# Kernel optimization log

Hardware: AMD Instinct MI355X
Metric: run time of the kernel (lower is better)

## Reference

```python
import jax, jax.numpy as jnp
import numpy as np

HIDDEN = 4544
NUM_HEADS = 71
HEAD_DIM = 64
SEQ = 2048
ROPE_BASE = 10000.0


def setup_inputs() -> dict:
    key = jax.random.key(0)
    k1, k2, k3 = jax.random.split(key, 3)
    hidden_states = jax.random.normal(k1, (1, 1, SEQ, HIDDEN), dtype=jnp.float32)
    # additive causal mask (0 on/below diagonal, -1e9 above)
    causal = jnp.tril(jnp.ones((SEQ, SEQ), dtype=bool))
    attention_mask = jnp.where(causal, 0.0, -1e9).astype(jnp.float32)[None, None]
    w_qkv = jax.random.normal(k2, (HIDDEN, (NUM_HEADS + 2) * HEAD_DIM), dtype=jnp.float32) * 0.02
    w_dense = jax.random.normal(k3, (HIDDEN, HIDDEN), dtype=jnp.float32) * 0.02
    # RoPE caches as in TtFalconRotaryEmbedding
    inv_freq = 1.0 / (ROPE_BASE ** (jnp.arange(0, HEAD_DIM, 2, dtype=jnp.float32) / HEAD_DIM))
    t = jnp.arange(SEQ, dtype=jnp.float32)
    freqs = jnp.outer(t, inv_freq)                      # [S, HD/2]
    emb = jnp.concatenate([freqs, freqs], axis=-1)      # [S, HD]
    return {
        "hidden_states": hidden_states,
        "attention_mask": attention_mask,
        "w_qkv": w_qkv,
        "w_dense": w_dense,
        "cos": jnp.cos(emb),
        "sin": jnp.sin(emb),
    }


def _rope(x, cos, sin):
    # x: [..., S, HD]; Falcon rotate_half: cat(-x2, x1)
    x1, x2 = jnp.split(x, 2, axis=-1)
    rot = jnp.concatenate([-x2, x1], axis=-1)
    return x * cos + rot * sin


def reference(hidden_states, attention_mask, w_qkv, w_dense, cos, sin):
    S = hidden_states.shape[2]
    x = hidden_states[0, 0]                              # [S, H]
    qkv = (x @ w_qkv).reshape(S, NUM_HEADS + 2, HEAD_DIM)
    q = jnp.transpose(qkv[:, :NUM_HEADS], (1, 0, 2))     # [nh, S, hd]
    k = qkv[:, NUM_HEADS]                                # [S, hd] (single MQA K head)
    v = qkv[:, NUM_HEADS + 1]                            # [S, hd]
    q = _rope(q, cos[None, :S], sin[None, :S])
    k = _rope(k, cos[:S], sin[:S])
    scale = 1.0 / np.sqrt(HEAD_DIM).astype(np.float32)
    scores = jnp.einsum('hsd,td->hst', q, k) * scale + attention_mask[0, 0][None]
    probs = jax.nn.softmax(scores, axis=-1)              # [nh, S, S]
    ctx = jnp.einsum('hst,td->hsd', probs, v)            # [nh, S, hd]
    out = jnp.transpose(ctx, (1, 0, 2)).reshape(S, NUM_HEADS * HEAD_DIM) @ w_dense
    return out[None, None]                               # [1, 1, S, H]
```

## Files before the change

### kernel.cpp

```cpp
#include <hip/hip_runtime.h>

typedef unsigned short u16;
typedef unsigned int u32;
typedef __attribute__((ext_vector_type(8))) __bf16 bf16x8;
typedef __attribute__((ext_vector_type(4))) float f32x4;

#define SEQ   2048
#define NH    71
#define HD    64
#define HID   4544
#define NQKV  4672
#define KP    4608

__device__ __forceinline__ u16 f2bf(float f) {
    __bf16 b = (__bf16)f;
    return __builtin_bit_cast(u16, b);
}

__device__ __forceinline__ void gload_lds16(const u16* g, u16* l) {
    __builtin_amdgcn_global_load_lds(
        (const __attribute__((address_space(1))) u32*)g,
        (__attribute__((address_space(3))) u32*)l, 16, 0, 0);
}

__global__ __launch_bounds__(256) void k_convert(const float* __restrict__ in,
                                                 u16* __restrict__ out) {
    const int row = blockIdx.x;
    const float* src = in + (size_t)row * HID;
    u16* dst = out + (size_t)row * KP;
    for (int c = threadIdx.x; c < KP / 8; c += 256) {
        u16 o[8];
        if (c < HID / 8) {
            float4 v0 = *(const float4*)(src + c * 8);
            float4 v1 = *(const float4*)(src + c * 8 + 4);
            o[0] = f2bf(v0.x); o[1] = f2bf(v0.y); o[2] = f2bf(v0.z); o[3] = f2bf(v0.w);
            o[4] = f2bf(v1.x); o[5] = f2bf(v1.y); o[6] = f2bf(v1.z); o[7] = f2bf(v1.w);
        } else {
#pragma unroll
            for (int j = 0; j < 8; ++j) o[j] = 0;
        }
        *(uint4*)(dst + c * 8) = *(uint4*)o;
    }
}

__global__ __launch_bounds__(256) void k_transpose(const float* __restrict__ in,
                                                   u16* __restrict__ out,
                                                   int R, int C, int Rp) {
    __shared__ float tile[32][33];
    int c0 = blockIdx.x * 32, r0 = blockIdx.y * 32;
    int tx = threadIdx.x & 31, ty = threadIdx.x >> 5;
#pragma unroll
    for (int i = 0; i < 32; i += 8) {
        int r = r0 + ty + i, c = c0 + tx;
        tile[ty + i][tx] = (r < R && c < C) ? in[(size_t)r * C + c] : 0.f;
    }
    __syncthreads();
#pragma unroll
    for (int i = 0; i < 32; i += 8)
        out[(size_t)(c0 + ty + i) * Rp + r0 + tx] = f2bf(tile[tx][ty + i]);
}

__global__ __launch_bounds__(512, 2) void k_gemm256(const u16* __restrict__ A,
                                                    const u16* __restrict__ BT,
                                                    float* __restrict__ C,
                                                    int N, int ldc) {
    __shared__ u16 lsA[2][256 * 64];
    __shared__ u16 lsB[2][256 * 64];
    const int tid = threadIdx.x;
    const int lane = tid & 63;
    const int wid = tid >> 6;
    const int wr = wid >> 2, wc = wid & 3;
    const int l15 = lane & 15, lg = lane >> 4;

    const int lin = blockIdx.y * gridDim.x + blockIdx.x;
    const int m0 = (lin & 7) * 256;
    const int n0 = (lin >> 3) * 256;

    const int srow = tid >> 3, sc = tid & 7;
    const u16* Ag = A + (size_t)(m0 + srow) * KP + (sc ^ (srow & 7)) * 8;
    const u16* Bg = BT + (size_t)(n0 + srow) * KP + (sc ^ (srow & 7)) * 8;

    f32x4 acc[8][4];
#pragma unroll
    for (int i = 0; i < 8; ++i)
#pragma unroll
        for (int j = 0; j < 4; ++j) acc[i][j] = (f32x4){0.f, 0.f, 0.f, 0.f};

#define STAGE(d, t)                                                                  \
    do {                                                                             \
        const size_t ko = (size_t)(t) * 64;                                          \
        _Pragma("unroll") for (int j = 0; j < 4; ++j)                                \
            gload_lds16(Ag + (size_t)j * 64 * KP + ko,                               \
                        lsA[d] + (j * 64 + srow) * 64 + sc * 8);                     \
        _Pragma("unroll") for (int j = 0; j < 4; ++j)                                \
            gload_lds16(Bg + (size_t)j * 64 * KP + ko,                               \
                        lsB[d] + (j * 64 + srow) * 64 + sc * 8);                     \
    } while (0)

    STAGE(0, 0);
    __syncthreads();

    const int NT = KP / 64;
    for (int t = 0; t < NT; ++t) {
        const int d = t & 1;
        if (t + 1 < NT) STAGE(d ^ 1, t + 1);
        const u16* La = lsA[d];
        const u16* Lb = lsB[d];
        bf16x8 bfr[4], af[4];
#pragma unroll
        for (int ni = 0; ni < 4; ++ni) {
            int r = wc * 64 + ni * 16 + l15;
            bfr[ni] = *(const bf16x8*)(Lb + r * 64 + ((lg ^ (r & 7)) << 3));
        }
#pragma unroll
        for (int mi = 0; mi < 4; ++mi) {
            int r = wr * 128 + mi * 16 + l15;
            af[mi] = *(const bf16x8*)(La + r * 64 + ((lg ^ (r & 7)) << 3));
        }
        __builtin_amdgcn_s_setprio(1);
#pragma unroll
        for (int mi = 0; mi < 4; ++mi)
#pragma unroll
            for (int ni = 0; ni < 4; ++ni)
                acc[mi][ni] = __builtin_amdgcn_mfma_f32_16x16x32_bf16(
                    af[mi], bfr[ni], acc[mi][ni], 0, 0, 0);
        __builtin_amdgcn_s_setprio(0);
        __builtin_amdgcn_s_barrier();
#pragma unroll
        for (int mi = 0; mi < 4; ++mi) {
            int r = wr * 128 + (mi + 4) * 16 + l15;
            af[mi] = *(const bf16x8*)(La + r * 64 + ((lg ^ (r & 7)) << 3));
        }
        __builtin_amdgcn_s_setprio(1);
#pragma unroll
        for (int mi = 0; mi < 4; ++mi)
#pragma unroll
            for (int ni = 0; ni < 4; ++ni)
                acc[mi + 4][ni] = __builtin_amdgcn_mfma_f32_16x16x32_bf16(
                    af[mi], bfr[ni], acc[mi + 4][ni], 0, 0, 0);
        __builtin_amdgcn_s_setprio(0);
        __builtin_amdgcn_s_barrier();
#pragma unroll
        for (int ni = 0; ni < 4; ++ni) {
            int r = wc * 64 + ni * 16 + l15;
            bfr[ni] = *(const bf16x8*)(Lb + r * 64 + (((4 + lg) ^ (r & 7)) << 3));
        }
#pragma unroll
        for (int mi = 0; mi < 4; ++mi) {
            int r = wr * 128 + mi * 16 + l15;
            af[mi] = *(const bf16x8*)(La + r * 64 + (((4 + lg) ^ (r & 7)) << 3));
        }
        __builtin_amdgcn_s_setprio(1);
#pragma unroll
        for (int mi = 0; mi < 4; ++mi)
#pragma unroll
            for (int ni = 0; ni < 4; ++ni)
                acc[mi][ni] = __builtin_amdgcn_mfma_f32_16x16x32_bf16(
                    af[mi], bfr[ni], acc[mi][ni], 0, 0, 0);
        __builtin_amdgcn_s_setprio(0);
        __builtin_amdgcn_s_barrier();
#pragma unroll
        for (int mi = 0; mi < 4; ++mi) {
            int r = wr * 128 + (mi + 4) * 16 + l15;
            af[mi] = *(const bf16x8*)(La + r * 64 + (((4 + lg) ^ (r & 7)) << 3));
        }
        __builtin_amdgcn_s_setprio(1);
#pragma unroll
        for (int mi = 0; mi < 4; ++mi)
#pragma unroll
            for (int ni = 0; ni < 4; ++ni)
                acc[mi + 4][ni] = __builtin_amdgcn_mfma_f32_16x16x32_bf16(
                    af[mi], bfr[ni], acc[mi + 4][ni], 0, 0, 0);
        __builtin_amdgcn_s_setprio(0);
        __syncthreads();
    }
#undef STAGE

#pragma unroll
    for (int mi = 0; mi < 8; ++mi)
#pragma unroll
        for (int ni = 0; ni < 4; ++ni) {
            int row = m0 + wr * 128 + mi * 16 + lg * 4;
            int col = n0 + wc * 64 + ni * 16 + l15;
            if (col < N) {
#pragma unroll
                for (int j = 0; j < 4; ++j)
                    C[(size_t)(row + j) * ldc + col] = acc[mi][ni][j];
            }
        }
}

__global__ __launch_bounds__(256) void k_rope(const float* __restrict__ qkv,
                                              const float* __restrict__ cosb,
                                              const float* __restrict__ sinb,
                                              u16* __restrict__ qb, u16* __restrict__ kb,
                                              u16* __restrict__ vT) {
    int s = blockIdx.x;
    __shared__ float cs[64], sn[64];
    if (threadIdx.x < 64) {
        cs[threadIdx.x] = cosb[s * 64 + threadIdx.x];
        sn[threadIdx.x] = sinb[s * 64 + threadIdx.x];
    }
    __syncthreads();
    const float* row = qkv + (size_t)s * NQKV;
    const float qscale = 0.125f * 1.44269504f;
    for (int e = threadIdx.x; e < NQKV; e += 256) {
        int h = e >> 6, d = e & 63;
        float x = row[e];
        if (h < 72) {
            float other = row[h * 64 + ((d < 32) ? d + 32 : d - 32)];
            float rot = (d < 32) ? -other : other;
            float r = x * cs[d] + rot * sn[d];
            if (h < NH) qb[((size_t)h * SEQ + s) * 64 + d] = f2bf(r * qscale);
            else        kb[(size_t)s * 64 + d] = f2bf(r);
        } else {
            vT[(size_t)d * SEQ + s] = f2bf(x);
        }
    }
}

__global__ __launch_bounds__(512) void k_attn(const u16* __restrict__ qb,
                                              const u16* __restrict__ kb,
                                              const u16* __restrict__ vT,
                                              u16* __restrict__ ctx) {
    const int tid = threadIdx.x;
    const int lane = tid & 63;
    const int wid = tid >> 6;
    const int l15 = lane & 15, lg = lane >> 4;

    const int bid = blockIdx.x;
    const int qt = 63 - bid / 9;
    const int hg = bid % 9;
    int h = hg * 8 + wid;
    const bool hval = (h < NH);
    if (!hval) h = NH - 1;
    const int q0 = qt * 32;
    const int nt = (qt >> 2) + 1;

    __shared__ u16 lsK[2][128 * 64];
    __shared__ u16 lsV[2][64 * 128];
    __shared__ u16 lsP[8][32 * 128];
    u16* myP = lsP[wid];

    const int kr = tid >> 3, kc = tid & 7;
    const int vd = tid >> 4, vc = tid & 15;

    bf16x8 qf[2][2];
#pragma unroll
    for (int mi = 0; mi < 2; ++mi)
#pragma unroll
        for (int ks = 0; ks < 2; ++ks)
            qf[mi][ks] = *(const bf16x8*)(qb + ((size_t)h * SEQ + q0 + mi * 16 + l15) * 64
                                          + ks * 32 + lg * 8);

    f32x4 oacc[2][4];
#pragma unroll
    for (int i = 0; i < 2; ++i)
#pragma unroll
        for (int j = 0; j < 4; ++j) oacc[i][j] = (f32x4){0.f, 0.f, 0.f, 0.f};
    float mrun[2] = {-3e38f, -3e38f};
    float lrun[2] = {0.f, 0.f};

    uint4 kg0, kg1, vg0, vg1;
    kg0 = *(const uint4*)(kb + (size_t)kr * 64 + kc * 8);
    kg1 = *(const uint4*)(kb + (size_t)(kr + 64) * 64 + kc * 8);
    vg0 = *(const uint4*)(vT + (size_t)vd * SEQ + vc * 8);
    vg1 = *(const uint4*)(vT + (size_t)(vd + 32) * SEQ + vc * 8);
    {
        const int kswz = (kr & 7) << 4;
        *(uint4*)((char*)lsK[0] + kr * 128 + ((kc * 16) ^ kswz)) = kg0;
        *(uint4*)((char*)lsK[0] + (kr + 64) * 128 + ((kc * 16) ^ kswz)) = kg1;
        *(uint4*)((char*)lsV[0] + vd * 256 + ((vc * 16) ^ ((vd & 15) << 4))) = vg0;
        *(uint4*)((char*)lsV[0] + (vd + 32) * 256 + ((vc * 16) ^ (((vd + 32) & 15) << 4))) = vg1;
    }

    for (int t = 0; t < nt; ++t) {
        const int t0 = t << 7;
        const int cb = t & 1;
        if (t + 1 < nt) {
            const int t1 = t0 + 128;
            kg0 = *(const uint4*)(kb + (size_t)(t1 + kr) * 64 + kc * 8);
            kg1 = *(const uint4*)(kb + (size_t)(t1 + kr + 64) * 64 + kc * 8);
            vg0 = *(const uint4*)(vT + (size_t)vd * SEQ + t1 + vc * 8);
            vg1 = *(const uint4*)(vT + (size_t)(vd + 32) * SEQ + t1 + vc * 8);
        }
        __syncthreads();

        f32x4 sacc[2][8];
#pragma unroll
        for (int i = 0; i < 2; ++i)
#pragma unroll
            for (int j = 0; j < 8; ++j) sacc[i][j] = (f32x4){0.f, 0.f, 0.f, 0.f};
#pragma unroll
        for (int ni = 0; ni < 8; ++ni) {
            const int r = ni * 16 + l15;
            const int swz = (r & 7) << 4;
            bf16x8 kf0 = *(const bf16x8*)((const char*)lsK[cb] + r * 128 + ((lg * 16) ^ swz));
            bf16x8 kf1 = *(const bf16x8*)((const char*)lsK[cb] + r * 128 + ((64 + lg * 16) ^ swz));
            sacc[0][ni] = __builtin_amdgcn_mfma_f32_16x16x32_bf16(kf0, qf[0][0], sacc[0][ni], 0, 0, 0);
            sacc[1][ni] = __builtin_amdgcn_mfma_f32_16x16x32_bf16(kf0, qf[1][0], sacc[1][ni], 0, 0, 0);
            sacc[0][ni] = __builtin_amdgcn_mfma_f32_16x16x32_bf16(kf1, qf[0][1], sacc[0][ni], 0, 0, 0);
            sacc[1][ni] = __builtin_amdgcn_mfma_f32_16x16x32_bf16(kf1, qf[1][1], sacc[1][ni], 0, 0, 0);
        }
        const bool last = (t == nt - 1);

#pragma unroll
        for (int mi = 0; mi < 2; ++mi) {
            const int q = q0 + mi * 16 + l15;
            if (last) {
#pragma unroll
                for (int ni = 0; ni < 8; ++ni)
#pragma unroll
                    for (int jj = 0; jj < 4; ++jj)
                        if (t0 + ni * 16 + lg * 4 + jj > q) sacc[mi][ni][jj] = -1e9f;
            }
            float m = sacc[mi][0][0];
#pragma unroll
            for (int ni = 0; ni < 8; ++ni)
#pragma unroll
                for (int jj = 0; jj < 4; ++jj) m = fmaxf(m, sacc[mi][ni][jj]);
            m = fmaxf(m, __shfl_xor(m, 16, 64));
            m = fmaxf(m, __shfl_xor(m, 32, 64));
            float mnew = fmaxf(mrun[mi], m);
            float alpha = exp2f(mrun[mi] - mnew);
            float rs = 0.f;
#pragma unroll
            for (int ni = 0; ni < 8; ++ni)
#pragma unroll
                for (int jj = 0; jj < 4; ++jj) {
                    float p = exp2f(sacc[mi][ni][jj] - mnew);
                    sacc[mi][ni][jj] = p;
                    rs += p;
                }
            rs += __shfl_xor(rs, 16, 64);
            rs += __shfl_xor(rs, 32, 64);
            lrun[mi] = lrun[mi] * alpha + rs;
            mrun[mi] = mnew;

            const int qh = mi * 16 + l15;
            const int pswz = (qh & 7) << 4;
#pragma unroll
            for (int ni = 0; ni < 8; ++ni) {
                u32 w0 = (u32)f2bf(sacc[mi][ni][0]) | ((u32)f2bf(sacc[mi][ni][1]) << 16);
                u32 w1 = (u32)f2bf(sacc[mi][ni][2]) | ((u32)f2bf(sacc[mi][ni][3]) << 16);
                uint2 w; w.x = w0; w.y = w1;
                *(uint2*)((char*)myP + qh * 256 + ((ni * 32 + lg * 8) ^ pswz)) = w;
            }
#pragma unroll
            for (int jj = 0; jj < 4; ++jj) {
                float aB = __shfl(alpha, (lane & 48) + ((lane >> 4) & 3) * 4 + jj, 64);
#pragma unroll
                for (int nd = 0; nd < 4; ++nd) oacc[mi][nd][jj] *= aB;
            }
        }

#pragma unroll
        for (int ks = 0; ks < 4; ++ks) {
            bf16x8 pf[2];
#pragma unroll
            for (int mi = 0; mi < 2; ++mi) {
                const int qh = mi * 16 + l15;
                pf[mi] = *(const bf16x8*)((const char*)myP + qh * 256
                                          + ((ks * 64 + lg * 16) ^ ((qh & 7) << 4)));
            }
#pragma unroll
            for (int nd = 0; nd < 4; ++nd) {
                const int r = nd * 16 + l15;
                bf16x8 vf = *(const bf16x8*)((const char*)lsV[cb] + r * 256
                                             + ((ks * 64 + lg * 16) ^ ((r & 15) << 4)));
                oacc[0][nd] = __builtin_amdgcn_mfma_f32_16x16x32_bf16(pf[0], vf, oacc[0][nd], 0, 0, 0);
                oacc[1][nd] = __builtin_amdgcn_mfma_f32_16x16x32_bf16(pf[1], vf, oacc[1][nd], 0, 0, 0);
            }
        }

        if (t + 1 < nt) {
            const int nb = cb ^ 1;
            const int kswz = (kr & 7) << 4;
            *(uint4*)((char*)lsK[nb] + kr * 128 + ((kc * 16) ^ kswz)) = kg0;
            *(uint4*)((char*)lsK[nb] + (kr + 64) * 128 + ((kc * 16) ^ kswz)) = kg1;
            *(uint4*)((char*)lsV[nb] + vd * 256 + ((vc * 16) ^ ((vd & 15) << 4))) = vg0;
            *(uint4*)((char*)lsV[nb] + (vd + 32) * 256 + ((vc * 16) ^ (((vd + 32) & 15) << 4))) = vg1;
        }
    }

    if (hval) {
#pragma unroll
        for (int mi = 0; mi < 2; ++mi)
#pragma unroll
            for (int jj = 0; jj < 4; ++jj) {
                float lB = __shfl(lrun[mi], (lane & 48) + ((lane >> 4) & 3) * 4 + jj, 64);
                float inv = 1.0f / lB;
                int q = q0 + mi * 16 + lg * 4 + jj;
#pragma unroll
                for (int nd = 0; nd < 4; ++nd)
                    ctx[(size_t)q * KP + h * 64 + nd * 16 + l15] = f2bf(oacc[mi][nd][jj] * inv);
            }
    } else {
#pragma unroll
        for (int mi = 0; mi < 2; ++mi)
#pragma unroll
            for (int jj = 0; jj < 4; ++jj) {
                int q = q0 + mi * 16 + lg * 4 + jj;
#pragma unroll
                for (int nd = 0; nd < 4; ++nd)
                    ctx[(size_t)q * KP + HID + nd * 16 + l15] = 0;
            }
    }
}

extern "C" void kernel_launch(void* const* d_in, const int* in_sizes, int n_in,
                              void* d_out, int out_size, void* d_ws, size_t ws_size,
                              hipStream_t stream) {
    const float* hs      = (const float*)d_in[0];
    const float* w_qkv   = (const float*)d_in[2];
    const float* w_dense = (const float*)d_in[3];
    const float* cosb    = (const float*)d_in[4];
    const float* sinb    = (const float*)d_in[5];
    float* out = (float*)d_out;

    char* ws = (char*)d_ws;
    u16*   x_bf  = (u16*)(ws + 0);
    u16*   wqkvT = (u16*)(ws + 18874368);
    float* qkv   = (float*)(ws + 63700992);
    u16*   q_bf  = (u16*)(ws + 101974016);
    u16*   k_bf  = (u16*)(ws + 120586240);
    u16*   vT_bf = (u16*)(ws + 120848384);
    u16*   wdenT = (u16*)(ws + 63700992);

    k_convert<<<2048, 256, 0, stream>>>(hs, x_bf);
    k_transpose<<<dim3(152, 144), 256, 0, stream>>>(w_qkv, wqkvT, HID, NQKV, KP);
    k_gemm256<<<dim3(19, 8), 512, 0, stream>>>(x_bf, wqkvT, qkv, NQKV, NQKV);
    k_rope<<<SEQ, 256, 0, stream>>>(qkv, cosb, sinb, q_bf, k_bf, vT_bf);
    k_attn<<<dim3(576), 512, 0, stream>>>(q_bf, k_bf, vT_bf, x_bf );
    k_transpose<<<dim3(144, 144), 256, 0, stream>>>(w_dense, wdenT, HID, HID, KP);
    k_gemm256<<<dim3(18, 8), 512, 0, stream>>>(x_bf , wdenT, out, HID, HID);
}
```

Measured before the change: 506.3 us.

## Split-K both GEMMs three ways with bf16 partials and finer-grained prefetch

Both projection GEMMs now split K into three 1536-wide slices, tripling the block count (456/432 instead of 152/144) so the 256x256 tiles fill the CU count better. The QKV partials are written as bf16 and summed inside the RoPE kernel. The dense partials are written as fp32 and summed by a new reduce kernel. The main loop's global->LDS prefetch is also split into four chunks interleaved between MFMA phases, with explicit vmcnt waits. This adds partial-buffer traffic, an extra kernel launch and bf16 rounding of the QKV partials.

Measured after the change: 516.3 us. About the same (+2.0%).

```diff
diff --git a/kernel.cpp b/kernel.cpp
--- a/kernel.cpp
+++ b/kernel.cpp
@@ -11,10 +11,15 @@
 #define HID   4544
 #define NQKV  4672
 #define KP    4608
+#define KSL   1536
 
 __device__ __forceinline__ u16 f2bf(float f) {
     __bf16 b = (__bf16)f;
     return __builtin_bit_cast(u16, b);
+}
+__device__ __forceinline__ float bf2f(u16 u) {
+    __bf16 b = __builtin_bit_cast(__bf16, u);
+    return (float)b;
 }
 
 __device__ __forceinline__ void gload_lds16(const u16* g, u16* l) {
@@ -60,10 +65,13 @@
         out[(size_t)(c0 + ty + i) * Rp + r0 + tx] = f2bf(tile[tx][ty + i]);
 }
 
-__global__ __launch_bounds__(512, 2) void k_gemm256(const u16* __restrict__ A,
-                                                    const u16* __restrict__ BT,
-                                                    float* __restrict__ C,
-                                                    int N, int ldc) {
+template <bool BF16OUT>
+__global__ __launch_bounds__(512) void k_gemm_sk(const u16* __restrict__ A,
+                                                 const u16* __restrict__ BT,
+                                                 char* __restrict__ C0,
+                                                 char* __restrict__ C1,
+                                                 char* __restrict__ C2,
+                                                 int N, int ntN) {
     __shared__ u16 lsA[2][256 * 64];
     __shared__ u16 lsB[2][256 * 64];
     const int tid = threadIdx.x;
@@ -72,13 +80,16 @@
     const int wr = wid >> 2, wc = wid & 3;
     const int l15 = lane & 15, lg = lane >> 4;
 
-    const int lin = blockIdx.y * gridDim.x + blockIdx.x;
-    const int m0 = (lin & 7) * 256;
-    const int n0 = (lin >> 3) * 256;
+    const int p = blockIdx.x;
+    const int m0 = (p & 7) * 256;
+    const int r = p >> 3;
+    const int ks = r / ntN;
+    const int n0 = (r % ntN) * 256;
+    const int k0 = ks * KSL;
 
     const int srow = tid >> 3, sc = tid & 7;
-    const u16* Ag = A + (size_t)(m0 + srow) * KP + (sc ^ (srow & 7)) * 8;
-    const u16* Bg = BT + (size_t)(n0 + srow) * KP + (sc ^ (srow & 7)) * 8;
+    const u16* Ag = A + (size_t)(m0 + srow) * KP + k0 + (sc ^ (srow & 7)) * 8;
+    const u16* Bg = BT + (size_t)(n0 + srow) * KP + k0 + (sc ^ (srow & 7)) * 8;
 
     f32x4 acc[8][4];
 #pragma unroll
@@ -86,36 +97,50 @@
 #pragma unroll
         for (int j = 0; j < 4; ++j) acc[i][j] = (f32x4){0.f, 0.f, 0.f, 0.f};
 
-#define STAGE(d, t)                                                                  \
-    do {                                                                             \
-        const size_t ko = (size_t)(t) * 64;                                          \
-        _Pragma("unroll") for (int j = 0; j < 4; ++j)                                \
-            gload_lds16(Ag + (size_t)j * 64 * KP + ko,                               \
-                        lsA[d] + (j * 64 + srow) * 64 + sc * 8);                     \
-        _Pragma("unroll") for (int j = 0; j < 4; ++j)                                \
-            gload_lds16(Bg + (size_t)j * 64 * KP + ko,                               \
-                        lsB[d] + (j * 64 + srow) * 64 + sc * 8);                     \
+#define CH_A(dst, ko, jb)                                                        \
+    do {                                                                         \
+        gload_lds16(Ag + (size_t)(jb) * 64 * KP + (ko),                          \
+                    lsA[dst] + ((jb) * 64 + srow) * 64 + sc * 8);                \
+        gload_lds16(Ag + (size_t)((jb) + 1) * 64 * KP + (ko),                    \
+                    lsA[dst] + (((jb) + 1) * 64 + srow) * 64 + sc * 8);          \
     } while (0)
-
-    STAGE(0, 0);
-    __syncthreads();
-
-    const int NT = KP / 64;
-    for (int t = 0; t < NT; ++t) {
-        const int d = t & 1;
-        if (t + 1 < NT) STAGE(d ^ 1, t + 1);
+#define CH_B(dst, ko, jb)                                                        \
+    do {                                                                         \
+        gload_lds16(Bg + (size_t)(jb) * 64 * KP + (ko),                          \
+                    lsB[dst] + ((jb) * 64 + srow) * 64 + sc * 8);                \
+        gload_lds16(Bg + (size_t)((jb) + 1) * 64 * KP + (ko),                    \
+                    lsB[dst] + (((jb) + 1) * 64 + srow) * 64 + sc * 8);          \
+    } while (0)
+
+    const int NT = KSL / 64;
+    CH_A(0, 0, 0); CH_A(0, 0, 2); CH_B(0, 0, 0); CH_B(0, 0, 2);
+
+    for (int kt = 0; kt < NT; ++kt) {
+        const int d = kt & 1;
+        const int nd = d ^ 1;
+        const size_t ko1 = (size_t)(kt + 1) * 64;
+        const bool st = (kt + 1 < NT);
         const u16* La = lsA[d];
         const u16* Lb = lsB[d];
         bf16x8 bfr[4], af[4];
+
+        if (st) {
+            CH_A(nd, ko1, 0);
+            asm volatile("s_waitcnt vmcnt(2)" ::: "memory");
+        } else {
+            asm volatile("s_waitcnt vmcnt(0)" ::: "memory");
+        }
+        __builtin_amdgcn_s_barrier();
+        __builtin_amdgcn_sched_barrier(0);
 #pragma unroll
         for (int ni = 0; ni < 4; ++ni) {
-            int r = wc * 64 + ni * 16 + l15;
-            bfr[ni] = *(const bf16x8*)(Lb + r * 64 + ((lg ^ (r & 7)) << 3));
+            int rr = wc * 64 + ni * 16 + l15;
+            bfr[ni] = *(const bf16x8*)(Lb + rr * 64 + ((lg ^ (rr & 7)) << 3));
         }
 #pragma unroll
         for (int mi = 0; mi < 4; ++mi) {
-            int r = wr * 128 + mi * 16 + l15;
-            af[mi] = *(const bf16x8*)(La + r * 64 + ((lg ^ (r & 7)) << 3));
+            int rr = wr * 128 + mi * 16 + l15;
+            af[mi] = *(const bf16x8*)(La + rr * 64 + ((lg ^ (rr & 7)) << 3));
         }
         __builtin_amdgcn_s_setprio(1);
 #pragma unroll
@@ -126,10 +151,12 @@
                     af[mi], bfr[ni], acc[mi][ni], 0, 0, 0);
         __builtin_amdgcn_s_setprio(0);
         __builtin_amdgcn_s_barrier();
+        __builtin_amdgcn_sched_barrier(0);
+        if (st) CH_A(nd, ko1, 2);
 #pragma unroll
         for (int mi = 0; mi < 4; ++mi) {
-            int r = wr * 128 + (mi + 4) * 16 + l15;
-            af[mi] = *(const bf16x8*)(La + r * 64 + ((lg ^ (r & 7)) << 3));
+            int rr = wr * 128 + (mi + 4) * 16 + l15;
+            af[mi] = *(const bf16x8*)(La + rr * 64 + ((lg ^ (rr & 7)) << 3));
         }
         __builtin_amdgcn_s_setprio(1);
 #pragma unroll
@@ -140,15 +167,17 @@
                     af[mi], bfr[ni], acc[mi + 4][ni], 0, 0, 0);
         __builtin_amdgcn_s_setprio(0);
         __builtin_amdgcn_s_barrier();
+        __builtin_amdgcn_sched_barrier(0);
+        if (st) CH_B(nd, ko1, 0);
 #pragma unroll
         for (int ni = 0; ni < 4; ++ni) {
-            int r = wc * 64 + ni * 16 + l15;
-            bfr[ni] = *(const bf16x8*)(Lb + r * 64 + (((4 + lg) ^ (r & 7)) << 3));
+            int rr = wc * 64 + ni * 16 + l15;
+            bfr[ni] = *(const bf16x8*)(Lb + rr * 64 + (((4 + lg) ^ (rr & 7)) << 3));
         }
 #pragma unroll
         for (int mi = 0; mi < 4; ++mi) {
-            int r = wr * 128 + mi * 16 + l15;
-            af[mi] = *(const bf16x8*)(La + r * 64 + (((4 + lg) ^ (r & 7)) << 3));
+            int rr = wr * 128 + mi * 16 + l15;
+            af[mi] = *(const bf16x8*)(La + rr * 64 + (((4 + lg) ^ (rr & 7)) << 3));
         }
         __builtin_amdgcn_s_setprio(1);
 #pragma unroll
@@ -159,10 +188,12 @@
                     af[mi], bfr[ni], acc[mi][ni], 0, 0, 0);
         __builtin_amdgcn_s_setprio(0);
         __builtin_amdgcn_s_barrier();
+        __builtin_amdgcn_sched_barrier(0);
+        if (st) CH_B(nd, ko1, 2);
 #pragma unroll
         for (int mi = 0; mi < 4; ++mi) {
-            int r = wr * 128 + (mi + 4) * 16 + l15;
-            af[mi] = *(const bf16x8*)(La + r * 64 + (((4 + lg) ^ (r & 7)) << 3));
+            int rr = wr * 128 + (mi + 4) * 16 + l15;
+            af[mi] = *(const bf16x8*)(La + rr * 64 + (((4 + lg) ^ (rr & 7)) << 3));
         }
         __builtin_amdgcn_s_setprio(1);
 #pragma unroll
@@ -172,10 +203,13 @@
                 acc[mi + 4][ni] = __builtin_amdgcn_mfma_f32_16x16x32_bf16(
                     af[mi], bfr[ni], acc[mi + 4][ni], 0, 0, 0);
         __builtin_amdgcn_s_setprio(0);
-        __syncthreads();
-    }
-#undef STAGE
-
+        __builtin_amdgcn_s_barrier();
+        __builtin_amdgcn_sched_barrier(0);
+    }
+#undef CH_A
+#undef CH_B
+
+    char* Cks = (ks == 0) ? C0 : (ks == 1) ? C1 : C2;
 #pragma unroll
     for (int mi = 0; mi < 8; ++mi)
 #pragma unroll
@@ -183,26 +217,53 @@
             int row = m0 + wr * 128 + mi * 16 + lg * 4;
             int col = n0 + wc * 64 + ni * 16 + l15;
             if (col < N) {
-#pragma unroll
-                for (int j = 0; j < 4; ++j)
-                    C[(size_t)(row + j) * ldc + col] = acc[mi][ni][j];
-            }
-        }
-}
-
-__global__ __launch_bounds__(256) void k_rope(const float* __restrict__ qkv,
+                if (BF16OUT) {
+                    u16* Cb = (u16*)Cks;
+#pragma unroll
+                    for (int j = 0; j < 4; ++j)
+                        Cb[(size_t)(row + j) * N + col] = f2bf(acc[mi][ni][j]);
+                } else {
+                    float* Cf = (float*)Cks;
+#pragma unroll
+                    for (int j = 0; j < 4; ++j)
+                        Cf[(size_t)(row + j) * N + col] = acc[mi][ni][j];
+                }
+            }
+        }
+}
+
+__global__ __launch_bounds__(256) void k_reduce(float* __restrict__ out,
+                                                const float* __restrict__ P1,
+                                                const float* __restrict__ P2, int n4) {
+    for (int i = blockIdx.x * 256 + threadIdx.x; i < n4; i += gridDim.x * 256) {
+        float4 a = ((const float4*)out)[i];
+        float4 b = ((const float4*)P1)[i];
+        float4 c = ((const float4*)P2)[i];
+        a.x += b.x + c.x; a.y += b.y + c.y; a.z += b.z + c.z; a.w += b.w + c.w;
+        ((float4*)out)[i] = a;
+    }
+}
+
+__global__ __launch_bounds__(256) void k_rope(const u16* __restrict__ P0,
+                                              const u16* __restrict__ P1,
+                                              const u16* __restrict__ P2,
                                               const float* __restrict__ cosb,
                                               const float* __restrict__ sinb,
                                               u16* __restrict__ qb, u16* __restrict__ kb,
                                               u16* __restrict__ vT) {
     int s = blockIdx.x;
+    __shared__ float row[NQKV];
     __shared__ float cs[64], sn[64];
     if (threadIdx.x < 64) {
         cs[threadIdx.x] = cosb[s * 64 + threadIdx.x];
         sn[threadIdx.x] = sinb[s * 64 + threadIdx.x];
     }
+    const u16* r0 = P0 + (size_t)s * NQKV;
+    const u16* r1 = P1 + (size_t)s * NQKV;
+    const u16* r2 = P2 + (size_t)s * NQKV;
+    for (int e = threadIdx.x; e < NQKV; e += 256)
+        row[e] = bf2f(r0[e]) + bf2f(r1[e]) + bf2f(r2[e]);
     __syncthreads();
-    const float* row = qkv + (size_t)s * NQKV;
     const float qscale = 0.125f * 1.44269504f;
     for (int e = threadIdx.x; e < NQKV; e += 256) {
         int h = e >> 6, d = e & 63;
@@ -210,9 +271,9 @@
         if (h < 72) {
             float other = row[h * 64 + ((d < 32) ? d + 32 : d - 32)];
             float rot = (d < 32) ? -other : other;
-            float r = x * cs[d] + rot * sn[d];
-            if (h < NH) qb[((size_t)h * SEQ + s) * 64 + d] = f2bf(r * qscale);
-            else        kb[(size_t)s * 64 + d] = f2bf(r);
+            float rr = x * cs[d] + rot * sn[d];
+            if (h < NH) qb[((size_t)h * SEQ + s) * 64 + d] = f2bf(rr * qscale);
+            else        kb[(size_t)s * 64 + d] = f2bf(rr);
         } else {
             vT[(size_t)d * SEQ + s] = f2bf(x);
         }
@@ -293,10 +354,10 @@
             for (int j = 0; j < 8; ++j) sacc[i][j] = (f32x4){0.f, 0.f, 0.f, 0.f};
 #pragma unroll
         for (int ni = 0; ni < 8; ++ni) {
-            const int r = ni * 16 + l15;
-            const int swz = (r & 7) << 4;
-            bf16x8 kf0 = *(const bf16x8*)((const char*)lsK[cb] + r * 128 + ((lg * 16) ^ swz));
-            bf16x8 kf1 = *(const bf16x8*)((const char*)lsK[cb] + r * 128 + ((64 + lg * 16) ^ swz));
+            const int rr = ni * 16 + l15;
+            const int swz = (rr & 7) << 4;
+            bf16x8 kf0 = *(const bf16x8*)((const char*)lsK[cb] + rr * 128 + ((lg * 16) ^ swz));
+            bf16x8 kf1 = *(const bf16x8*)((const char*)lsK[cb] + rr * 128 + ((64 + lg * 16) ^ swz));
             sacc[0][ni] = __builtin_amdgcn_mfma_f32_16x16x32_bf16(kf0, qf[0][0], sacc[0][ni], 0, 0, 0);
             sacc[1][ni] = __builtin_amdgcn_mfma_f32_16x16x32_bf16(kf0, qf[1][0], sacc[1][ni], 0, 0, 0);
             sacc[0][ni] = __builtin_amdgcn_mfma_f32_16x16x32_bf16(kf1, qf[0][1], sacc[0][ni], 0, 0, 0);
@@ -328,9 +389,9 @@
             for (int ni = 0; ni < 8; ++ni)
 #pragma unroll
                 for (int jj = 0; jj < 4; ++jj) {
-                    float p = exp2f(sacc[mi][ni][jj] - mnew);
-                    sacc[mi][ni][jj] = p;
-                    rs += p;
+                    float pp = exp2f(sacc[mi][ni][jj] - mnew);
+                    sacc[mi][ni][jj] = pp;
+                    rs += pp;
                 }
             rs += __shfl_xor(rs, 16, 64);
             rs += __shfl_xor(rs, 32, 64);
@@ -365,9 +426,9 @@
             }
 #pragma unroll
             for (int nd = 0; nd < 4; ++nd) {
-                const int r = nd * 16 + l15;
-                bf16x8 vf = *(const bf16x8*)((const char*)lsV[cb] + r * 256
-                                             + ((ks * 64 + lg * 16) ^ ((r & 15) << 4)));
+                const int rr = nd * 16 + l15;
+                bf16x8 vf = *(const bf16x8*)((const char*)lsV[cb] + rr * 256
+                                             + ((ks * 64 + lg * 16) ^ ((rr & 15) << 4)));
                 oacc[0][nd] = __builtin_amdgcn_mfma_f32_16x16x32_bf16(pf[0], vf, oacc[0][nd], 0, 0, 0);
                 oacc[1][nd] = __builtin_amdgcn_mfma_f32_16x16x32_bf16(pf[1], vf, oacc[1][nd], 0, 0, 0);
             }
@@ -420,18 +481,25 @@
 
     char* ws = (char*)d_ws;
     u16*   x_bf  = (u16*)(ws + 0);
-    u16*   wqkvT = (u16*)(ws + 18874368);
-    float* qkv   = (float*)(ws + 63700992);
-    u16*   q_bf  = (u16*)(ws + 101974016);
-    u16*   k_bf  = (u16*)(ws + 120586240);
-    u16*   vT_bf = (u16*)(ws + 120848384);
-    u16*   wdenT = (u16*)(ws + 63700992);
+    u16*   wT    = (u16*)(ws + 18874368);
+    char*  qP0   = ws + 63700992;
+    char*  qP1   = ws + 82837504;
+    char*  qP2   = ws + 101974016;
+    u16*   q_bf  = (u16*)(ws + 121110528);
+    u16*   k_bf  = (u16*)(ws + 139722752);
+    u16*   vT_bf = (u16*)(ws + 139984896);
+    char*  dP1   = ws + 63700992;
+    char*  dP2   = ws + 100925440;
 
     k_convert<<<2048, 256, 0, stream>>>(hs, x_bf);
-    k_transpose<<<dim3(152, 144), 256, 0, stream>>>(w_qkv, wqkvT, HID, NQKV, KP);
-    k_gemm256<<<dim3(19, 8), 512, 0, stream>>>(x_bf, wqkvT, qkv, NQKV, NQKV);
-    k_rope<<<SEQ, 256, 0, stream>>>(qkv, cosb, sinb, q_bf, k_bf, vT_bf);
+    k_transpose<<<dim3(152, 144), 256, 0, stream>>>(w_qkv, wT, HID, NQKV, KP);
+    k_gemm_sk<true><<<dim3(456), 512, 0, stream>>>(x_bf, wT, qP0, qP1, qP2, NQKV, 19);
+    k_rope<<<SEQ, 256, 0, stream>>>((const u16*)qP0, (const u16*)qP1, (const u16*)qP2,
+                                    cosb, sinb, q_bf, k_bf, vT_bf);
     k_attn<<<dim3(576), 512, 0, stream>>>(q_bf, k_bf, vT_bf, x_bf );
-    k_transpose<<<dim3(144, 144), 256, 0, stream>>>(w_dense, wdenT, HID, HID, KP);
-    k_gemm256<<<dim3(18, 8), 512, 0, stream>>>(x_bf , wdenT, out, HID, HID);
-}
+    k_transpose<<<dim3(144, 144), 256, 0, stream>>>(w_dense, wT, HID, HID, KP);
+    k_gemm_sk<false><<<dim3(432), 512, 0, stream>>>(x_bf , wT,
+                                                    (char*)out, dP1, dP2, HID, 18);
+    k_reduce<<<2048, 256, 0, stream>>>(out, (const float*)dP1, (const float*)dP2,
+                                       SEQ * HID / 4);
+}
```
